# Kernel optimization log

Measured on AMD Instinct MI355X. Metric: run time of the kernel, lower is better.

Reference implementation:

```python
import jax, jax.numpy as jnp
import numpy as np

B, T, D, H = 1, 2048, 1024, 16
DH = D // H
DFF = 4 * D
SPARSITY_LAMBDA = 0.0005
LN_EPS = 1e-5


def _ln(x, g, b):
    mu = jnp.mean(x, axis=-1, keepdims=True)
    var = jnp.mean((x - mu) ** 2, axis=-1, keepdims=True)
    return (x - mu) * jax.lax.rsqrt(var + LN_EPS) * g + b


def setup_inputs() -> dict:
    key = jax.random.key(0)
    ks = jax.random.split(key, 8)
    s = lambda fan: 1.0 / np.sqrt(fan)
    inp = {
        "x": jax.random.normal(ks[0], (B, T, D), jnp.float32),
        "causal_mask": jnp.triu(jnp.ones((T, T), jnp.bool_), 1),
        "W_qkv": jax.random.normal(ks[1], (3 * D, D), jnp.float32) * s(D),
        "W_out": jax.random.normal(ks[2], (D, D), jnp.float32) * s(D),
        "log_mask": jnp.zeros((1, H, T, T), jnp.float32),
        "W_gate": jax.random.normal(ks[3], (D, 2 * D), jnp.float32) * s(2 * D),
        "b_gate": jnp.zeros((D,), jnp.float32),
        "g1": jnp.ones((D,), jnp.float32),
        "b1": jnp.zeros((D,), jnp.float32),
        "g2": jnp.ones((D,), jnp.float32),
        "b2": jnp.zeros((D,), jnp.float32),
        "W_ff1": jax.random.normal(ks[4], (DFF, D), jnp.float32) * s(D),
        "b_ff1": jnp.zeros((DFF,), jnp.float32),
        "W_ff2": jax.random.normal(ks[5], (D, DFF), jnp.float32) * s(DFF),
        "b_ff2": jnp.zeros((D,), jnp.float32),
    }
    return inp


def reference(x, causal_mask, W_qkv, W_out, log_mask, W_gate, b_gate,
              g1, b1, g2, b2, W_ff1, b_ff1, W_ff2, b_ff2):
    Bx, Tx, Dx = x.shape
    xn = _ln(x, g1, b1)
    qkv = xn @ W_qkv.T                              # [B,T,3D]
    q, k, v = jnp.split(qkv, 3, axis=-1)
    rs = lambda t: t.reshape(Bx, Tx, H, DH).transpose(0, 2, 1, 3)  # [B,H,T,dh]
    q, k, v = rs(q), rs(k), rs(v)
    scale = jnp.sqrt(jnp.asarray(DH, x.dtype))
    qk = jnp.einsum("bhtd,bhsd->bhts", q, k) / scale  # [B,H,T,T]
    cm = causal_mask[:Tx, :Tx]
    neg = jnp.asarray(-jnp.inf, x.dtype)
    # stream 1: plain causal softmax
    a_txt = jax.nn.softmax(jnp.where(cm, neg, qk), axis=-1)
    out_txt = jnp.einsum("bhts,bhsd->bhtd", a_txt, v)
    # stream 2: sigmoid-gated scores then causal softmax
    M = jax.nn.sigmoid(log_mask[:, :, :Tx, :Tx])
    a_cau = jax.nn.softmax(jnp.where(cm, neg, qk * M), axis=-1)
    out_cau = jnp.einsum("bhts,bhsd->bhtd", a_cau, v)
    merge = lambda t: t.transpose(0, 2, 1, 3).reshape(Bx, Tx, Dx)
    cat = jnp.concatenate([merge(out_txt), merge(out_cau)], axis=-1)  # [B,T,2D]
    a = (cat @ W_gate.T + b_gate) @ W_out.T
    sp = SPARSITY_LAMBDA * jnp.mean(M)
    # residual + FFN (dropout=0, eval mode)
    h = x + a
    hn = _ln(h, g2, b2)
    ff = jax.nn.gelu(hn @ W_ff1.T + b_ff1, approximate=False) @ W_ff2.T + b_ff2
    return h + ff, sp
```

## Files before the change

kernel.cpp:

```cpp
#include <hip/hip_runtime.h>
#include <hip/hip_bf16.h>

typedef __bf16 bf16x8 __attribute__((ext_vector_type(8)));
typedef _Float16 f16x4 __attribute__((ext_vector_type(4)));
typedef float f32x4 __attribute__((ext_vector_type(4)));

#define MFMA16(a, b, c) __builtin_amdgcn_mfma_f32_16x16x32_bf16(a, b, c, 0, 0, 0)
#define MFMA16H(a, b, c) __builtin_amdgcn_mfma_f32_16x16x16f16(a, b, c, 0, 0, 0)

#define T_SEQ 2048
#define D_MODEL 1024
#define N_HEADS 16
#define HEAD_DIM 64
#define D_FF 4096
#define QKV_STRIDE 3072

__device__ __forceinline__ float sigm(float x) { return 1.f / (1.f + __expf(-x)); }

__device__ __forceinline__ void g2l16(const void* g, void* l)
{
    __builtin_amdgcn_global_load_lds(
        (const __attribute__((address_space(1))) void*)g,
        (__attribute__((address_space(3))) void*)l, 16, 0, 0);
}

__device__ __forceinline__ float bperm(int srclane, float v)
{
    return __builtin_bit_cast(float,
        __builtin_amdgcn_ds_bpermute(srclane * 4, __builtin_bit_cast(int, v)));
}

#define N8_QKV 393216
#define N8_OUT 131072
#define N8_GATE 262144
#define N8_FF1 524288
#define N8_FF2 524288
__global__ __launch_bounds__(256) void cast_all_kernel(
    const float* __restrict__ s0, const float* __restrict__ s1,
    const float* __restrict__ s2, const float* __restrict__ s3,
    const float* __restrict__ s4,
    __bf16* __restrict__ d0, __bf16* __restrict__ d1, __bf16* __restrict__ d2,
    __bf16* __restrict__ d3, __bf16* __restrict__ d4)
{
    int i = blockIdx.x * 256 + threadIdx.x;
    const float* s; __bf16* d; int j;
    if (i < N8_QKV)                           { s = s0; d = d0; j = i; }
    else if (i < N8_QKV + N8_OUT)             { s = s1; d = d1; j = i - N8_QKV; }
    else if (i < N8_QKV + N8_OUT + N8_GATE)   { s = s2; d = d2; j = i - N8_QKV - N8_OUT; }
    else if (i < N8_QKV + N8_OUT + N8_GATE + N8_FF1)
        { s = s3; d = d3; j = i - N8_QKV - N8_OUT - N8_GATE; }
    else { s = s4; d = d4; j = i - N8_QKV - N8_OUT - N8_GATE - N8_FF1; }
    const float4* p = (const float4*)s + (size_t)j * 2;
    float4 a = p[0], b = p[1];
    union { __bf16 h[8]; float4 v; } u;
    u.h[0] = (__bf16)a.x; u.h[1] = (__bf16)a.y; u.h[2] = (__bf16)a.z; u.h[3] = (__bf16)a.w;
    u.h[4] = (__bf16)b.x; u.h[5] = (__bf16)b.y; u.h[6] = (__bf16)b.z; u.h[7] = (__bf16)b.w;
    ((float4*)d)[j] = u.v;
}

__global__ __launch_bounds__(256) void ln_kernel(
    const float* __restrict__ x, const float* __restrict__ g,
    const float* __restrict__ b, __bf16* __restrict__ out)
{
    const int t = blockIdx.x;
    const int tid = threadIdx.x;
    float4 xv = *(const float4*)&x[t * D_MODEL + tid * 4];
    float s = xv.x + xv.y + xv.z + xv.w;
    float ss = xv.x * xv.x + xv.y * xv.y + xv.z * xv.z + xv.w * xv.w;
    for (int off = 1; off < 64; off <<= 1) {
        s += __shfl_xor(s, off);
        ss += __shfl_xor(ss, off);
    }
    __shared__ float sb[8];
    int w = tid >> 6, lane = tid & 63;
    if (lane == 0) { sb[w] = s; sb[4 + w] = ss; }
    __syncthreads();
    s = sb[0] + sb[1] + sb[2] + sb[3];
    ss = sb[4] + sb[5] + sb[6] + sb[7];
    float mu = s * (1.f / D_MODEL);
    float var = ss * (1.f / D_MODEL) - mu * mu;
    float rs = rsqrtf(var + 1e-5f);
    const float* xp = (const float*)&xv;
    for (int i = 0; i < 4; ++i) {
        int d = tid * 4 + i;
        out[t * D_MODEL + d] = (__bf16)((xp[i] - mu) * rs * g[d] + b[d]);
    }
}

template<int BM, int EPI>
__global__ __launch_bounds__(256) void gemm_nt(
    const __bf16* __restrict__ A, const __bf16* __restrict__ B,
    const float* __restrict__ bias,
    __bf16* __restrict__ outb, float* __restrict__ outf,
    int M, int N, int klen, int lda)
{
    constexpr int BN = 128;
    constexpr int EOUT = (EPI == 3) ? 4 : 2;
    constexpr int STAGE = (BM + BN) * 64 * 2;
    constexpr int CTB = BM * BN * EOUT;
    constexpr int SMEM = (STAGE > CTB) ? STAGE : CTB;
    __shared__ __align__(16) char smem[SMEM];
    __bf16* As = (__bf16*)smem;
    __bf16* Bs = As + BM * 64;

    const int tid = threadIdx.x;
    const int lane = tid & 63, w = tid >> 6;
    const int quad = lane >> 4, l16 = lane & 15;
    const int bm = blockIdx.x * BM, bn = blockIdx.y * BN;
    const int koff = blockIdx.z * klen;
    if (EPI == 3) outf += (size_t)blockIdx.z * M * N;
    constexpr int NI = 4;
    constexpr int NJ = (BM == 128) ? 4 : 2;
    const int wm = (BM == 128) ? (w & 1) * 64 : 0;
    const int wn = (BM == 128) ? (w >> 1) * 64 : w * 32;

    f32x4 acc[NI][NJ] = {};

    for (int k0 = 0; k0 < klen; k0 += 64) {
        __syncthreads();
        constexpr int AIT = BM * 8 / 256;
        for (int it = 0; it < AIT; ++it) {
            int c = it * 256 + tid;
            int tile = (c >= BM * 4) ? 1 : 0;
            int c2 = c & (BM * 4 - 1);
            g2l16(&A[(size_t)(bm + (c2 >> 2)) * lda + koff + k0 + tile * 32 + ((c2 & 3) << 3)],
                  &As[c * 8]);
        }
        for (int it = 0; it < 4; ++it) {
            int c = it * 256 + tid;
            int tile = (c >= 512) ? 1 : 0;
            int c2 = c & 511;
            g2l16(&B[(size_t)(bn + (c2 >> 2)) * lda + koff + k0 + tile * 32 + ((c2 & 3) << 3)],
                  &Bs[c * 8]);
        }
        __syncthreads();
        for (int ks = 0; ks < 2; ++ks) {
            bf16x8 af[NI], bfr[NJ];
            for (int i = 0; i < NI; ++i)
                af[i] = *(const bf16x8*)&As[ks * BM * 32 + (wm + i * 16 + l16) * 32 + quad * 8];
            for (int j = 0; j < NJ; ++j)
                bfr[j] = *(const bf16x8*)&Bs[ks * BN * 32 + (wn + j * 16 + l16) * 32 + quad * 8];
            for (int i = 0; i < NI; ++i)
                for (int j = 0; j < NJ; ++j)
                    acc[i][j] = MFMA16(af[i], bfr[j], acc[i][j]);
        }
    }

    __syncthreads();
    if (EPI == 3) {
        float* Ct = (float*)smem;
        for (int i = 0; i < NI; ++i)
            for (int j = 0; j < NJ; ++j)
                for (int r = 0; r < 4; ++r)
                    Ct[(wm + i * 16 + quad * 4 + r) * BN + wn + j * 16 + l16] = acc[i][j][r];
        __syncthreads();
        constexpr int IT = BM * BN / 4 / 256;
        for (int it = 0; it < IT; ++it) {
            int c = it * 256 + tid;
            int row = c >> 5, col = (c & 31) << 2;
            *(float4*)&outf[(size_t)(bm + row) * N + bn + col] = *(float4*)&Ct[row * BN + col];
        }
    } else {
        __bf16* Ct = (__bf16*)smem;
        for (int i = 0; i < NI; ++i)
            for (int j = 0; j < NJ; ++j)
                for (int r = 0; r < 4; ++r) {
                    int row = wm + i * 16 + quad * 4 + r;
                    int col = wn + j * 16 + l16;
                    float v = acc[i][j][r];
                    if (bias) v += bias[bn + col];
                    if (EPI == 1) v = 0.5f * v * (1.f + erff(v * 0.70710678118f));
                    Ct[row * BN + col] = (__bf16)v;
                }
        __syncthreads();
        constexpr int IT = BM * BN / 8 / 256;
        for (int it = 0; it < IT; ++it) {
            int c = it * 256 + tid;
            int row = c >> 4, col = (c & 15) << 3;
            *(float4*)&outb[(size_t)(bm + row) * N + bn + col] = *(float4*)&Ct[row * BN + col];
        }
    }
}

template<int MODE>
__global__ __launch_bounds__(256) void combine_kernel(
    const float* __restrict__ p0, const float* __restrict__ p1,
    const float* __restrict__ bias, const float* __restrict__ resid,
    __bf16* __restrict__ outb, float* __restrict__ outf)
{
    int i = blockIdx.x * 256 + threadIdx.x;
    float4 a = ((const float4*)p0)[i];
    float4 b = ((const float4*)p1)[i];
    float v[4] = {a.x + b.x, a.y + b.y, a.z + b.z, a.w + b.w};
    if (MODE == 0 || MODE == 2) {
        int col = (i & 255) << 2;
        float4 bb = *(const float4*)&bias[col];
        v[0] += bb.x; v[1] += bb.y; v[2] += bb.z; v[3] += bb.w;
    }
    if (MODE >= 1) {
        float4 r = ((const float4*)resid)[i];
        v[0] += r.x; v[1] += r.y; v[2] += r.z; v[3] += r.w;
    }
    if (MODE == 0) {
        union { __bf16 h[4]; float2 f2; } u;
        for (int e = 0; e < 4; ++e) u.h[e] = (__bf16)v[e];
        ((float2*)outb)[i] = u.f2;
    } else {
        float4 o = {v[0], v[1], v[2], v[3]};
        ((float4*)outf)[i] = o;
    }
}

__global__ __launch_bounds__(256) void vtrans_kernel(
    const __bf16* __restrict__ qkv, _Float16* __restrict__ vt)
{
    __shared__ __bf16 Vl[64 * 72];
    const int t0 = blockIdx.x * 64, h = blockIdx.y;
    const int tid = threadIdx.x;
    for (int it = 0; it < 2; ++it) {
        int c = it * 256 + tid;
        int row = c >> 3, col8 = (c & 7) << 3;
        *(float4*)&Vl[row * 72 + col8] =
            *(const float4*)&qkv[(size_t)(t0 + row) * QKV_STRIDE + 2048 + h * 64 + col8];
    }
    __syncthreads();
    int d = tid >> 2, tseg = (tid & 3) << 4;
    _Float16 buf[16];
    for (int i = 0; i < 16; ++i)
        buf[i] = (_Float16)(float)Vl[(tseg + i) * 72 + d];
    _Float16* dst = &vt[((size_t)h * 64 + d) * T_SEQ + t0 + tseg];
    *(float4*)&dst[0] = *(float4*)&buf[0];
    *(float4*)&dst[8] = *(float4*)&buf[8];
}

__global__ __launch_bounds__(256) void attn_split_kernel(
    const __bf16* __restrict__ qkv, const _Float16* __restrict__ vt,
    const float* __restrict__ lmask,
    __bf16* __restrict__ part_O, float2* __restrict__ part_ml,
    float* __restrict__ sigacc)
{
    __shared__ __bf16 Ks[2 * 64 * 32];
    __shared__ _Float16 Vs[64 * 64];

    const int tid = threadIdx.x;
    const int w = tid >> 6, lane = tid & 63;
    const int quad = lane >> 4, l16 = lane & 15;
    const int idx = blockIdx.x, h = blockIdx.y;
    int qt, sp;
    if (idx < 8)       { qt = idx;                sp = 0; }
    else if (idx < 24) { qt = 8 + ((idx - 8) >> 1);  sp = (idx - 8) & 1; }
    else if (idx < 48) { qt = 16 + (idx - 24) / 3;   sp = (idx - 24) % 3; }
    else               { qt = 24 + ((idx - 48) >> 2); sp = (idx - 48) & 3; }
    const int q0 = qt * 64;
    const int sbeg = sp * 512;
    const int send = min(sbeg + 512, q0 + 64);

    const int tq = q0 + w * 16 + l16;
    bf16x8 qf0 = *(const bf16x8*)&qkv[(size_t)tq * QKV_STRIDE + h * 64 + quad * 8];
    bf16x8 qf1 = *(const bf16x8*)&qkv[(size_t)tq * QKV_STRIDE + h * 64 + 32 + quad * 8];

    float m_[2] = {-1e30f, -1e30f}, l_[2] = {0.f, 0.f};
    f32x4 O[2][4] = {};
    float sigsum = 0.f;

    for (int s0 = sbeg; s0 < send; s0 += 64) {
        float4 lm[4];
        for (int c = 0; c < 4; ++c)
            lm[c] = *(const float4*)&lmask[((size_t)h * T_SEQ + tq) * T_SEQ + s0 + c * 16 + quad * 4];
        __syncthreads();
        for (int it = 0; it < 2; ++it) {
            int c = it * 256 + tid;
            int tile = c >> 8, c2 = c & 255;
            g2l16(&qkv[(size_t)(s0 + (c2 >> 2)) * QKV_STRIDE + 1024 + h * 64 + tile * 32 + ((c2 & 3) << 3)],
                  &Ks[c * 8]);
        }
        for (int it = 0; it < 2; ++it) {
            int c = it * 256 + tid;
            int dh = c >> 3, g = c & 7;
            int sIn = ((g + dh) & 7) * 8;
            g2l16(&vt[((size_t)h * 64 + dh) * T_SEQ + s0 + sIn], &Vs[c * 8]);
        }
        __syncthreads();

        f32x4 St[4];
        for (int c = 0; c < 4; ++c) {
            bf16x8 kf0 = *(const bf16x8*)&Ks[(c * 16 + l16) * 32 + quad * 8];
            bf16x8 kf1 = *(const bf16x8*)&Ks[2048 + (c * 16 + l16) * 32 + quad * 8];
            f32x4 z = {};
            z = MFMA16(kf0, qf0, z);
            z = MFMA16(kf1, qf1, z);
            St[c] = z * 0.125f;
        }
        f16x4 vf[4][4];
        for (int c = 0; c < 4; ++c)
            for (int j = 0; j < 4; ++j) {
                int dh = j * 16 + l16;
                int gg = ((2 * c + (quad >> 1)) - dh) & 7;
                vf[c][j] = *(const f16x4*)&Vs[dh * 64 + gg * 8 + (quad & 1) * 4];
            }
        float sg[4][4];
        for (int c = 0; c < 4; ++c) {
            const float* lp = (const float*)&lm[c];
            for (int r = 0; r < 4; ++r) { sg[c][r] = sigm(lp[r]); sigsum += sg[c][r]; }
        }

        for (int v = 0; v < 2; ++v) {
            float p[4][4];
            float mx = -1e30f;
            for (int c = 0; c < 4; ++c) {
                int sbase = s0 + c * 16 + quad * 4;
                for (int r = 0; r < 4; ++r) {
                    float val = v ? St[c][r] * sg[c][r] : St[c][r];
                    val = (sbase + r > tq) ? -1e30f : val;
                    p[c][r] = val;
                    mx = fmaxf(mx, val);
                }
            }
            mx = fmaxf(mx, __shfl_xor(mx, 16));
            mx = fmaxf(mx, __shfl_xor(mx, 32));
            float mn = fmaxf(m_[v], mx);
            float al = __expf(m_[v] - mn);
            m_[v] = mn;
            float rs = 0.f;
            f16x4 pa[4];
            for (int c = 0; c < 4; ++c)
                for (int r = 0; r < 4; ++r) {
                    float e = __expf(p[c][r] - mn);
                    rs += e;
                    pa[c][r] = (_Float16)e;
                }
            rs += __shfl_xor(rs, 16);
            rs += __shfl_xor(rs, 32);
            l_[v] = l_[v] * al + rs;
            float alO[4];
            for (int r = 0; r < 4; ++r) alO[r] = bperm(quad * 4 + r, al);
            for (int j = 0; j < 4; ++j)
                for (int r = 0; r < 4; ++r) O[v][j][r] *= alO[r];
            for (int c = 0; c < 4; ++c)
                for (int j = 0; j < 4; ++j)
                    O[v][j] = MFMA16H(pa[c], vf[c][j], O[v][j]);
        }
    }

    const size_t slot = (size_t)h * 80 + idx;
    for (int v = 0; v < 2; ++v)
        for (int j = 0; j < 4; ++j)
            for (int r = 0; r < 4; ++r) {
                int row = w * 16 + quad * 4 + r;
                part_O[((slot * 2 + v) * 64 + row) * 64 + j * 16 + l16] = (__bf16)O[v][j][r];
            }
    if (quad == 0)
        for (int v = 0; v < 2; ++v)
            part_ml[(slot * 2 + v) * 64 + w * 16 + l16] = make_float2(m_[v], l_[v]);
    for (int off = 1; off < 64; off <<= 1) sigsum += __shfl_xor(sigsum, off);
    if (lane == 0) atomicAdd(sigacc, sigsum);
}

__global__ __launch_bounds__(256) void attn_combine_kernel(
    const __bf16* __restrict__ part_O, const float2* __restrict__ part_ml,
    __bf16* __restrict__ cat)
{
    const int qt = blockIdx.x, h = blockIdx.y;
    const int nsp = (qt >> 3) + 1;
    const int base = (qt < 8) ? qt : (qt < 16) ? 8 + (qt - 8) * 2
                   : (qt < 24) ? 24 + (qt - 16) * 3 : 48 + (qt - 24) * 4;
    const int tid = threadIdx.x;
    const int row = tid >> 2, v = (tid >> 1) & 1, colh = (tid & 1) * 32;

    float2 ml[4];
    float M = -1e30f;
    for (int p = 0; p < nsp; ++p) {
        ml[p] = part_ml[(((size_t)h * 80 + base + p) * 2 + v) * 64 + row];
        M = fmaxf(M, ml[p].x);
    }
    float L = 0.f;
    float acc[32] = {};
    for (int p = 0; p < nsp; ++p) {
        float sc = __expf(ml[p].x - M);
        L += sc * ml[p].y;
        const __bf16* src =
            &part_O[((((size_t)h * 80 + base + p) * 2 + v) * 64 + row) * 64 + colh];
        for (int k = 0; k < 4; ++k) {
            bf16x8 o = *(const bf16x8*)&src[k * 8];
            for (int e = 0; e < 8; ++e) acc[k * 8 + e] += sc * (float)o[e];
        }
    }
    float inv = 1.f / L;
    __bf16* dst = &cat[(size_t)(qt * 64 + row) * 2048 + v * 1024 + h * 64 + colh];
    for (int k = 0; k < 4; ++k) {
        union { __bf16 hh[8]; float4 f4; } u;
        for (int e = 0; e < 8; ++e) u.hh[e] = (__bf16)(acc[k * 8 + e] * inv);
        *(float4*)&dst[k * 8] = u.f4;
    }
}

__global__ void zero_acc_kernel(float* acc) { acc[0] = 0.f; }

__global__ __launch_bounds__(256) void sigmean_upper_kernel(
    const float* __restrict__ lm, float* __restrict__ acc)
{
    const int qt = blockIdx.x, h = blockIdx.y, rg = blockIdx.z;
    const int sc0 = (qt + 1) * 64;
    const int len4 = (T_SEQ - sc0) >> 2;
    float s = 0.f;
    for (int r = 0; r < 16; ++r) {
        const float* rowp = &lm[((size_t)h * T_SEQ + qt * 64 + rg * 16 + r) * T_SEQ + sc0];
        for (int c = threadIdx.x; c < len4; c += 256) {
            float4 a = *(const float4*)&rowp[c * 4];
            s += sigm(a.x) + sigm(a.y) + sigm(a.z) + sigm(a.w);
        }
    }
    for (int off = 1; off < 64; off <<= 1) s += __shfl_xor(s, off);
    if ((threadIdx.x & 63) == 0) atomicAdd(acc, s);
}

__global__ void write_sp_kernel(const float* __restrict__ acc, float* __restrict__ out)
{
    out[(size_t)T_SEQ * D_MODEL] = 0.0005f * acc[0] * (1.f / 67108864.f);
}

extern "C" void kernel_launch(void* const* d_in, const int* in_sizes, int n_in,
                              void* d_out, int out_size, void* d_ws, size_t ws_size,
                              hipStream_t stream)
{
    const float* x      = (const float*)d_in[0];
    const float* W_qkv  = (const float*)d_in[2];
    const float* W_out  = (const float*)d_in[3];
    const float* lmask  = (const float*)d_in[4];
    const float* W_gate = (const float*)d_in[5];
    const float* b_gate = (const float*)d_in[6];
    const float* g1     = (const float*)d_in[7];
    const float* b1     = (const float*)d_in[8];
    const float* g2     = (const float*)d_in[9];
    const float* b2     = (const float*)d_in[10];
    const float* W_ff1  = (const float*)d_in[11];
    const float* b_ff1  = (const float*)d_in[12];
    const float* W_ff2  = (const float*)d_in[13];
    const float* b_ff2  = (const float*)d_in[14];
    float* out = (float*)d_out;

    char* ws = (char*)d_ws;
    size_t off = 0;
    auto alloc = [&](size_t bytes) {
        char* p = ws + off;
        off += (bytes + 255) & ~(size_t)255;
        return p;
    };
    __bf16* wq_b   = (__bf16*)alloc((size_t)3072 * 1024 * 2);
    __bf16* wout_b = (__bf16*)alloc((size_t)1024 * 1024 * 2);
    __bf16* wg_b   = (__bf16*)alloc((size_t)1024 * 2048 * 2);
    __bf16* wf1_b  = (__bf16*)alloc((size_t)4096 * 1024 * 2);
    __bf16* wf2_b  = (__bf16*)alloc((size_t)1024 * 4096 * 2);
    __bf16* xn_b   = (__bf16*)alloc((size_t)2048 * 1024 * 2);
    __bf16* qkv_b  = (__bf16*)alloc((size_t)2048 * 3072 * 2);
    _Float16* vt_h = (_Float16*)alloc((size_t)16 * 64 * 2048 * 2);
    __bf16* cat_b  = (__bf16*)alloc((size_t)2048 * 2048 * 2);
    __bf16* a1_b   = (__bf16*)alloc((size_t)2048 * 1024 * 2);
    float*  h_f    = (float*)alloc((size_t)2048 * 1024 * 4);
    __bf16* hn_b   = (__bf16*)alloc((size_t)2048 * 1024 * 2);
    __bf16* e_b    = (__bf16*)alloc((size_t)2048 * 4096 * 2);
    __bf16* part_O = (__bf16*)alloc((size_t)16 * 80 * 2 * 64 * 64 * 2);
    float2* part_ml= (float2*)alloc((size_t)16 * 80 * 2 * 64 * 8);
    float*  psum   = (float*)alloc((size_t)2 * 2048 * 1024 * 4);
    float*  acc    = (float*)alloc(256);
    float*  psum1  = psum + (size_t)2048 * 1024;

    zero_acc_kernel<<<1, 1, 0, stream>>>(acc);

    cast_all_kernel<<<7168, 256, 0, stream>>>(W_qkv, W_out, W_gate, W_ff1, W_ff2,
                                              wq_b, wout_b, wg_b, wf1_b, wf2_b);

    ln_kernel<<<2048, 256, 0, stream>>>(x, g1, b1, xn_b);
    gemm_nt<64, 0><<<dim3(32, 24), 256, 0, stream>>>(xn_b, wq_b, nullptr, qkv_b, nullptr, 2048, 3072, 1024, 1024);
    vtrans_kernel<<<dim3(32, 16), 256, 0, stream>>>(qkv_b, vt_h);
    attn_split_kernel<<<dim3(80, 16), 256, 0, stream>>>(qkv_b, vt_h, lmask, part_O, part_ml, acc);
    attn_combine_kernel<<<dim3(32, 16), 256, 0, stream>>>(part_O, part_ml, cat_b);
    sigmean_upper_kernel<<<dim3(32, 16, 4), 256, 0, stream>>>(lmask, acc);

    gemm_nt<64, 3><<<dim3(32, 8, 2), 256, 0, stream>>>(cat_b, wg_b, nullptr, nullptr, psum, 2048, 1024, 1024, 2048);
    combine_kernel<0><<<2048, 256, 0, stream>>>(psum, psum1, b_gate, nullptr, a1_b, nullptr);
    gemm_nt<64, 3><<<dim3(32, 8, 2), 256, 0, stream>>>(a1_b, wout_b, nullptr, nullptr, psum, 2048, 1024, 512, 1024);
    combine_kernel<1><<<2048, 256, 0, stream>>>(psum, psum1, nullptr, x, nullptr, h_f);
    ln_kernel<<<2048, 256, 0, stream>>>(h_f, g2, b2, hn_b);
    gemm_nt<128, 1><<<dim3(16, 32), 256, 0, stream>>>(hn_b, wf1_b, b_ff1, e_b, nullptr, 2048, 4096, 1024, 1024);
    gemm_nt<64, 3><<<dim3(32, 8, 2), 256, 0, stream>>>(e_b, wf2_b, nullptr, nullptr, psum, 2048, 1024, 2048, 4096);
    combine_kernel<2><<<2048, 256, 0, stream>>>(psum, psum1, b_ff2, h_f, nullptr, out);

    write_sp_kernel<<<1, 1, 0, stream>>>(acc, out);

    (void)in_sizes; (void)n_in; (void)out_size; (void)ws_size;
}
```

Baseline: 782.5 us.

## Fuse V-transpose, sigmoid-mean, LN2, and tiny kernels; double-buffer attention K/V staging

Several small kernels are folded into their neighbours. The V transpose moves into the QKV GEMM epilogue, the upper-triangle sigmoid mean into the attention kernel, and the second LayerNorm into the residual combine. The accumulator zeroing goes into the cast kernel and the sparsity write into the final combine. The attention split kernel now double-buffers its K/V LDS tiles so the next chunk's loads overlap compute. The intent is to cut launch overhead and extra global passes over qkv, h and log_mask. In exchange LDS use and register pressure go up, and a combine now adds the bias in every mode, so mode 1 would read a null pointer, though it is no longer launched.

```diff
diff --git a/kernel.cpp b/kernel.cpp
--- a/kernel.cpp
+++ b/kernel.cpp
@@ -40,9 +40,10 @@
     const float* __restrict__ s2, const float* __restrict__ s3,
     const float* __restrict__ s4,
     __bf16* __restrict__ d0, __bf16* __restrict__ d1, __bf16* __restrict__ d2,
-    __bf16* __restrict__ d3, __bf16* __restrict__ d4)
+    __bf16* __restrict__ d3, __bf16* __restrict__ d4, float* __restrict__ acc)
 {
     int i = blockIdx.x * 256 + threadIdx.x;
+    if (i == 0) acc[0] = 0.f;
     const float* s; __bf16* d; int j;
     if (i < N8_QKV)                           { s = s0; d = d0; j = i; }
     else if (i < N8_QKV + N8_OUT)             { s = s1; d = d1; j = i - N8_QKV; }
@@ -91,13 +92,12 @@
 __global__ __launch_bounds__(256) void gemm_nt(
     const __bf16* __restrict__ A, const __bf16* __restrict__ B,
     const float* __restrict__ bias,
-    __bf16* __restrict__ outb, float* __restrict__ outf,
+    __bf16* __restrict__ outb, float* __restrict__ outf, _Float16* __restrict__ vtout,
     int M, int N, int klen, int lda)
 {
     constexpr int BN = 128;
-    constexpr int EOUT = (EPI == 3) ? 4 : 2;
     constexpr int STAGE = (BM + BN) * 64 * 2;
-    constexpr int CTB = BM * BN * EOUT;
+    constexpr int CTB = (EPI == 3) ? BM * BN * 4 : (EPI == 4) ? BM * 132 * 4 : BM * BN * 2;
     constexpr int SMEM = (STAGE > CTB) ? STAGE : CTB;
     __shared__ __align__(16) char smem[SMEM];
     __bf16* As = (__bf16*)smem;
@@ -159,6 +159,35 @@
             int c = it * 256 + tid;
             int row = c >> 5, col = (c & 31) << 2;
             *(float4*)&outf[(size_t)(bm + row) * N + bn + col] = *(float4*)&Ct[row * BN + col];
+        }
+    } else if (EPI == 4) {
+        float* Ct = (float*)smem;
+        for (int i = 0; i < NI; ++i)
+            for (int j = 0; j < NJ; ++j)
+                for (int r = 0; r < 4; ++r)
+                    Ct[(wm + i * 16 + quad * 4 + r) * 132 + wn + j * 16 + l16] = acc[i][j][r];
+        __syncthreads();
+        if (bn < 2048) {
+            for (int it = 0; it < BM * BN / 8 / 256; ++it) {
+                int c = it * 256 + tid;
+                int row = c >> 4, col8 = (c & 15) << 3;
+                float4 f0 = *(float4*)&Ct[row * 132 + col8];
+                float4 f1 = *(float4*)&Ct[row * 132 + col8 + 4];
+                union { __bf16 h[8]; float4 v; } u;
+                u.h[0] = (__bf16)f0.x; u.h[1] = (__bf16)f0.y; u.h[2] = (__bf16)f0.z; u.h[3] = (__bf16)f0.w;
+                u.h[4] = (__bf16)f1.x; u.h[5] = (__bf16)f1.y; u.h[6] = (__bf16)f1.z; u.h[7] = (__bf16)f1.w;
+                *(float4*)&outb[(size_t)(bm + row) * N + bn + col8] = u.v;
+            }
+        } else {
+            int col = tid & 127;
+            int r0 = (tid >> 7) * 32;
+            int gcol = bn - 2048 + col;
+            _Float16 buf[32];
+            for (int r = 0; r < 32; ++r)
+                buf[r] = (_Float16)Ct[(r0 + r) * 132 + col];
+            _Float16* dst = &vtout[(size_t)gcol * T_SEQ + bm + r0];
+            for (int k = 0; k < 4; ++k)
+                *(float4*)&dst[k * 8] = *(float4*)&buf[k * 8];
         }
     } else {
         __bf16* Ct = (__bf16*)smem;
@@ -186,51 +215,64 @@
 __global__ __launch_bounds__(256) void combine_kernel(
     const float* __restrict__ p0, const float* __restrict__ p1,
     const float* __restrict__ bias, const float* __restrict__ resid,
-    __bf16* __restrict__ outb, float* __restrict__ outf)
+    __bf16* __restrict__ outb, float* __restrict__ outf,
+    const float* __restrict__ sigacc)
 {
     int i = blockIdx.x * 256 + threadIdx.x;
     float4 a = ((const float4*)p0)[i];
     float4 b = ((const float4*)p1)[i];
-    float v[4] = {a.x + b.x, a.y + b.y, a.z + b.z, a.w + b.w};
-    if (MODE == 0 || MODE == 2) {
-        int col = (i & 255) << 2;
-        float4 bb = *(const float4*)&bias[col];
-        v[0] += bb.x; v[1] += bb.y; v[2] += bb.z; v[3] += bb.w;
-    }
-    if (MODE >= 1) {
+    int col = (i & 255) << 2;
+    float4 bb = *(const float4*)&bias[col];
+    float v[4] = {a.x + b.x + bb.x, a.y + b.y + bb.y, a.z + b.z + bb.z, a.w + b.w + bb.w};
+    if (MODE == 2) {
         float4 r = ((const float4*)resid)[i];
         v[0] += r.x; v[1] += r.y; v[2] += r.z; v[3] += r.w;
-    }
-    if (MODE == 0) {
+        float4 o = {v[0], v[1], v[2], v[3]};
+        ((float4*)outf)[i] = o;
+        if (i == 0)
+            outf[(size_t)T_SEQ * D_MODEL] = 0.0005f * sigacc[0] * (1.f / 67108864.f);
+    } else {
         union { __bf16 h[4]; float2 f2; } u;
         for (int e = 0; e < 4; ++e) u.h[e] = (__bf16)v[e];
         ((float2*)outb)[i] = u.f2;
-    } else {
-        float4 o = {v[0], v[1], v[2], v[3]};
-        ((float4*)outf)[i] = o;
-    }
-}
-
-__global__ __launch_bounds__(256) void vtrans_kernel(
-    const __bf16* __restrict__ qkv, _Float16* __restrict__ vt)
-{
-    __shared__ __bf16 Vl[64 * 72];
-    const int t0 = blockIdx.x * 64, h = blockIdx.y;
-    const int tid = threadIdx.x;
-    for (int it = 0; it < 2; ++it) {
-        int c = it * 256 + tid;
-        int row = c >> 3, col8 = (c & 7) << 3;
-        *(float4*)&Vl[row * 72 + col8] =
-            *(const float4*)&qkv[(size_t)(t0 + row) * QKV_STRIDE + 2048 + h * 64 + col8];
-    }
+    }
+}
+
+__global__ __launch_bounds__(256) void combine_ln_kernel(
+    const float* __restrict__ p0, const float* __restrict__ p1,
+    const float* __restrict__ resid, const float* __restrict__ g,
+    const float* __restrict__ b, float* __restrict__ h_out,
+    __bf16* __restrict__ hn_out)
+{
+    const int t = blockIdx.x, tid = threadIdx.x;
+    const int i = t * 256 + tid;
+    float4 a = ((const float4*)p0)[i];
+    float4 bb = ((const float4*)p1)[i];
+    float4 r = ((const float4*)resid)[i];
+    float4 v = {a.x + bb.x + r.x, a.y + bb.y + r.y, a.z + bb.z + r.z, a.w + bb.w + r.w};
+    ((float4*)h_out)[i] = v;
+    float s = v.x + v.y + v.z + v.w;
+    float ss = v.x * v.x + v.y * v.y + v.z * v.z + v.w * v.w;
+    for (int off = 1; off < 64; off <<= 1) {
+        s += __shfl_xor(s, off);
+        ss += __shfl_xor(ss, off);
+    }
+    __shared__ float sb[8];
+    int w = tid >> 6, lane = tid & 63;
+    if (lane == 0) { sb[w] = s; sb[4 + w] = ss; }
     __syncthreads();
-    int d = tid >> 2, tseg = (tid & 3) << 4;
-    _Float16 buf[16];
-    for (int i = 0; i < 16; ++i)
-        buf[i] = (_Float16)(float)Vl[(tseg + i) * 72 + d];
-    _Float16* dst = &vt[((size_t)h * 64 + d) * T_SEQ + t0 + tseg];
-    *(float4*)&dst[0] = *(float4*)&buf[0];
-    *(float4*)&dst[8] = *(float4*)&buf[8];
+    s = sb[0] + sb[1] + sb[2] + sb[3];
+    ss = sb[4] + sb[5] + sb[6] + sb[7];
+    float mu = s * (1.f / D_MODEL);
+    float var = ss * (1.f / D_MODEL) - mu * mu;
+    float rs = rsqrtf(var + 1e-5f);
+    const float* vp = (const float*)&v;
+    union { __bf16 h[4]; float2 f2; } u;
+    for (int k = 0; k < 4; ++k) {
+        int d = tid * 4 + k;
+        u.h[k] = (__bf16)((vp[k] - mu) * rs * g[d] + b[d]);
+    }
+    ((float2*)hn_out)[i] = u.f2;
 }
 
 __global__ __launch_bounds__(256) void attn_split_kernel(
@@ -239,8 +281,8 @@
     __bf16* __restrict__ part_O, float2* __restrict__ part_ml,
     float* __restrict__ sigacc)
 {
-    __shared__ __bf16 Ks[2 * 64 * 32];
-    __shared__ _Float16 Vs[64 * 64];
+    __shared__ __bf16 KsAll[2 * 4096];
+    __shared__ _Float16 VsAll[2 * 4096];
 
     const int tid = threadIdx.x;
     const int w = tid >> 6, lane = tid & 63;
@@ -254,33 +296,54 @@
     const int q0 = qt * 64;
     const int sbeg = sp * 512;
     const int send = min(sbeg + 512, q0 + 64);
-
-    const int tq = q0 + w * 16 + l16;
-    bf16x8 qf0 = *(const bf16x8*)&qkv[(size_t)tq * QKV_STRIDE + h * 64 + quad * 8];
-    bf16x8 qf1 = *(const bf16x8*)&qkv[(size_t)tq * QKV_STRIDE + h * 64 + 32 + quad * 8];
-
-    float m_[2] = {-1e30f, -1e30f}, l_[2] = {0.f, 0.f};
-    f32x4 O[2][4] = {};
-    float sigsum = 0.f;
-
-    for (int s0 = sbeg; s0 < send; s0 += 64) {
-        float4 lm[4];
-        for (int c = 0; c < 4; ++c)
-            lm[c] = *(const float4*)&lmask[((size_t)h * T_SEQ + tq) * T_SEQ + s0 + c * 16 + quad * 4];
-        __syncthreads();
+    const int nch = (send - sbeg) >> 6;
+
+    auto stage = [&](int s0, int bsel) {
+        __bf16* kd = &KsAll[bsel * 4096];
+        _Float16* vd = &VsAll[bsel * 4096];
         for (int it = 0; it < 2; ++it) {
             int c = it * 256 + tid;
             int tile = c >> 8, c2 = c & 255;
             g2l16(&qkv[(size_t)(s0 + (c2 >> 2)) * QKV_STRIDE + 1024 + h * 64 + tile * 32 + ((c2 & 3) << 3)],
-                  &Ks[c * 8]);
+                  &kd[c * 8]);
         }
         for (int it = 0; it < 2; ++it) {
             int c = it * 256 + tid;
             int dh = c >> 3, g = c & 7;
             int sIn = ((g + dh) & 7) * 8;
-            g2l16(&vt[((size_t)h * 64 + dh) * T_SEQ + s0 + sIn], &Vs[c * 8]);
-        }
+            g2l16(&vt[((size_t)h * 64 + dh) * T_SEQ + s0 + sIn], &vd[c * 8]);
+        }
+    };
+
+    const int tq = q0 + w * 16 + l16;
+    bf16x8 qf0 = *(const bf16x8*)&qkv[(size_t)tq * QKV_STRIDE + h * 64 + quad * 8];
+    bf16x8 qf1 = *(const bf16x8*)&qkv[(size_t)tq * QKV_STRIDE + h * 64 + 32 + quad * 8];
+
+    float m_[2] = {-1e30f, -1e30f}, l_[2] = {0.f, 0.f};
+    f32x4 O[2][4] = {};
+    float sigsum = 0.f;
+
+    stage(sbeg, 0);
+
+    for (int ci = 0; ci < nch; ++ci) {
+        const int s0 = sbeg + (ci << 6);
+        const int cur = ci & 1;
         __syncthreads();
+
+        float4 lm[4];
+        for (int c = 0; c < 4; ++c)
+            lm[c] = *(const float4*)&lmask[((size_t)h * T_SEQ + tq) * T_SEQ + s0 + c * 16 + quad * 4];
+        float4 up[4];
+        const bool lower = (s0 + 64 <= q0);
+        if (lower) {
+            const float* upp = &lmask[((size_t)h * T_SEQ + s0 + (tid >> 2)) * T_SEQ + q0 + ((tid & 3) << 4)];
+            for (int k = 0; k < 4; ++k) up[k] = *(const float4*)&upp[k * 4];
+        }
+
+        if (ci + 1 < nch) stage(s0 + 64, cur ^ 1);
+
+        const __bf16* Ks = &KsAll[cur * 4096];
+        const _Float16* Vs = &VsAll[cur * 4096];
 
         f32x4 St[4];
         for (int c = 0; c < 4; ++c) {
@@ -297,6 +360,12 @@
                 int dh = j * 16 + l16;
                 int gg = ((2 * c + (quad >> 1)) - dh) & 7;
                 vf[c][j] = *(const f16x4*)&Vs[dh * 64 + gg * 8 + (quad & 1) * 4];
+            }
+
+        if (lower)
+            for (int k = 0; k < 4; ++k) {
+                const float* uu = (const float*)&up[k];
+                sigsum += sigm(uu[0]) + sigm(uu[1]) + sigm(uu[2]) + sigm(uu[3]);
             }
         float sg[4][4];
         for (int c = 0; c < 4; ++c) {
@@ -394,31 +463,6 @@
     }
 }
 
-__global__ void zero_acc_kernel(float* acc) { acc[0] = 0.f; }
-
-__global__ __launch_bounds__(256) void sigmean_upper_kernel(
-    const float* __restrict__ lm, float* __restrict__ acc)
-{
-    const int qt = blockIdx.x, h = blockIdx.y, rg = blockIdx.z;
-    const int sc0 = (qt + 1) * 64;
-    const int len4 = (T_SEQ - sc0) >> 2;
-    float s = 0.f;
-    for (int r = 0; r < 16; ++r) {
-        const float* rowp = &lm[((size_t)h * T_SEQ + qt * 64 + rg * 16 + r) * T_SEQ + sc0];
-        for (int c = threadIdx.x; c < len4; c += 256) {
-            float4 a = *(const float4*)&rowp[c * 4];
-            s += sigm(a.x) + sigm(a.y) + sigm(a.z) + sigm(a.w);
-        }
-    }
-    for (int off = 1; off < 64; off <<= 1) s += __shfl_xor(s, off);
-    if ((threadIdx.x & 63) == 0) atomicAdd(acc, s);
-}
-
-__global__ void write_sp_kernel(const float* __restrict__ acc, float* __restrict__ out)
-{
-    out[(size_t)T_SEQ * D_MODEL] = 0.0005f * acc[0] * (1.f / 67108864.f);
-}
-
 extern "C" void kernel_launch(void* const* d_in, const int* in_sizes, int n_in,
                               void* d_out, int out_size, void* d_ws, size_t ws_size,
                               hipStream_t stream)
@@ -465,28 +509,19 @@
     float*  acc    = (float*)alloc(256);
     float*  psum1  = psum + (size_t)2048 * 1024;
 
-    zero_acc_kernel<<<1, 1, 0, stream>>>(acc);
-
     cast_all_kernel<<<7168, 256, 0, stream>>>(W_qkv, W_out, W_gate, W_ff1, W_ff2,
-                                              wq_b, wout_b, wg_b, wf1_b, wf2_b);
-
+                                              wq_b, wout_b, wg_b, wf1_b, wf2_b, acc);
     ln_kernel<<<2048, 256, 0, stream>>>(x, g1, b1, xn_b);
-    gemm_nt<64, 0><<<dim3(32, 24), 256, 0, stream>>>(xn_b, wq_b, nullptr, qkv_b, nullptr, 2048, 3072, 1024, 1024);
-    vtrans_kernel<<<dim3(32, 16), 256, 0, stream>>>(qkv_b, vt_h);
+    gemm_nt<64, 4><<<dim3(32, 24), 256, 0, stream>>>(xn_b, wq_b, nullptr, qkv_b, nullptr, vt_h, 2048, 3072, 1024, 1024);
     attn_split_kernel<<<dim3(80, 16), 256, 0, stream>>>(qkv_b, vt_h, lmask, part_O, part_ml, acc);
     attn_combine_kernel<<<dim3(32, 16), 256, 0, stream>>>(part_O, part_ml, cat_b);
-    sigmean_upper_kernel<<<dim3(32, 16, 4), 256, 0, stream>>>(lmask, acc);
-
-    gemm_nt<64, 3><<<dim3(32, 8, 2), 256, 0, stream>>>(cat_b, wg_b, nullptr, nullptr, psum, 2048, 1024, 1024, 2048);
-    combine_kernel<0><<<2048, 256, 0, stream>>>(psum, psum1, b_gate, nullptr, a1_b, nullptr);
-    gemm_nt<64, 3><<<dim3(32, 8, 2), 256, 0, stream>>>(a1_b, wout_b, nullptr, nullptr, psum, 2048, 1024, 512, 1024);
-    combine_kernel<1><<<2048, 256, 0, stream>>>(psum, psum1, nullptr, x, nullptr, h_f);
-    ln_kernel<<<2048, 256, 0, stream>>>(h_f, g2, b2, hn_b);
-    gemm_nt<128, 1><<<dim3(16, 32), 256, 0, stream>>>(hn_b, wf1_b, b_ff1, e_b, nullptr, 2048, 4096, 1024, 1024);
-    gemm_nt<64, 3><<<dim3(32, 8, 2), 256, 0, stream>>>(e_b, wf2_b, nullptr, nullptr, psum, 2048, 1024, 2048, 4096);
-    combine_kernel<2><<<2048, 256, 0, stream>>>(psum, psum1, b_ff2, h_f, nullptr, out);
-
-    write_sp_kernel<<<1, 1, 0, stream>>>(acc, out);
+    gemm_nt<64, 3><<<dim3(32, 8, 2), 256, 0, stream>>>(cat_b, wg_b, nullptr, nullptr, psum, nullptr, 2048, 1024, 1024, 2048);
+    combine_kernel<0><<<2048, 256, 0, stream>>>(psum, psum1, b_gate, nullptr, a1_b, nullptr, nullptr);
+    gemm_nt<64, 3><<<dim3(32, 8, 2), 256, 0, stream>>>(a1_b, wout_b, nullptr, nullptr, psum, nullptr, 2048, 1024, 512, 1024);
+    combine_ln_kernel<<<2048, 256, 0, stream>>>(psum, psum1, x, g2, b2, h_f, hn_b);
+    gemm_nt<128, 1><<<dim3(16, 32), 256, 0, stream>>>(hn_b, wf1_b, b_ff1, e_b, nullptr, nullptr, 2048, 4096, 1024, 1024);
+    gemm_nt<64, 3><<<dim3(32, 8, 2), 256, 0, stream>>>(e_b, wf2_b, nullptr, nullptr, psum, nullptr, 2048, 1024, 2048, 4096);
+    combine_kernel<2><<<2048, 256, 0, stream>>>(psum, psum1, b_ff2, h_f, nullptr, out, acc);
 
     (void)in_sizes; (void)n_in; (void)out_size; (void)ws_size;
 }
```

Result: faster. 667.6 us (-14.7%).
